# Optimization experiments

Measured on AMD Instinct MI355X. Metric: run time of the kernel, lower is better.

The kernel has to match this reference:

```python
import jax, jax.numpy as jnp
import numpy as np


def setup_inputs() -> dict:
    key = jax.random.key(0)
    k1, k2, k3, k4 = jax.random.split(key, 4)
    B, T, H = 4, 512, 256
    scale = 1.0 / np.sqrt(H)
    return {
        "rnn_outputs": jax.random.normal(k1, (B, T, H), dtype=jnp.float32),
        "W1": jax.random.normal(k2, (H, H), dtype=jnp.float32) * scale,
        "W2": jax.random.normal(k3, (H, H), dtype=jnp.float32) * scale,
        "v": jax.random.normal(k4, (H,), dtype=jnp.float32) * scale,
    }


def reference(rnn_outputs, W1, W2, v):
    """Bahdanau additive self-attention with causal mask.

    rnn_outputs: (B, T, H). Returns (context (B,T,H), weights (B,T,T)).
    """
    B, T, H = rnn_outputs.shape
    # nn.Linear applies x @ W.T
    query = rnn_outputs @ W1.T            # (B, T, H)
    keys = rnn_outputs @ W2.T             # (B, T, H)
    # scores[b,t,s] = v . tanh(q[b,t] + k[b,s]); materializes (B,T,T,H) like the original
    scores = jnp.einsum(
        "btsh,h->bts", jnp.tanh(query[:, :, None, :] + keys[:, None, :, :]), v
    )
    causal = jnp.triu(jnp.ones((T, T), dtype=bool), k=1)  # mask future positions
    scores = jnp.where(causal[None], -jnp.inf, scores)
    weights = jax.nn.softmax(scores, axis=-1)
    weights = jnp.nan_to_num(weights)
    context = jnp.einsum("bts,bsh->bth", weights, rnn_outputs)
    return context, weights
```

## Files before the change

### kernel.cpp

```cpp
#include <hip/hip_runtime.h>

namespace {

constexpr int kB = 4;
constexpr int kT = 512;
constexpr int kH = 256;

__device__ __forceinline__ float rcpf(float x) {
  return __builtin_amdgcn_rcpf(x);
}

__global__ __launch_bounds__(256) void transpose_w_kernel(
    const float* __restrict__ W1, const float* __restrict__ W2,
    float* __restrict__ Wt1, float* __restrict__ Wt2) {
  __shared__ float tile[32][33];
  const float* Win = (blockIdx.z == 0) ? W1 : W2;
  float* Wout = (blockIdx.z == 0) ? Wt1 : Wt2;
  const int jo = blockIdx.x * 32, ho = blockIdx.y * 32;
  const int c = threadIdx.x & 31, r0 = threadIdx.x >> 5;
#pragma unroll
  for (int p = 0; p < 4; ++p)
    tile[r0 + 8 * p][c] = Win[(size_t)(ho + r0 + 8 * p) * kH + jo + c];
  __syncthreads();
#pragma unroll
  for (int p = 0; p < 4; ++p)
    Wout[(size_t)(jo + r0 + 8 * p) * kH + ho + c] = tile[c][r0 + 8 * p];
}

__global__ __launch_bounds__(256) void proj_kernel(
    const float* __restrict__ X, const float* __restrict__ Wt1,
    const float* __restrict__ Wt2, float* __restrict__ EQt,
    float* __restrict__ EKt) {
  __shared__ __align__(16) float ws4[4][16][kH];

  const int tid = threadIdx.x;
  const int w = tid >> 6, lane = tid & 63;
  const int row0 = blockIdx.x * 8;
  const float* Wt = (blockIdx.y == 0) ? Wt1 : Wt2;
  float* dst = (blockIdx.y == 0) ? EQt : EKt;

  const float* gw = Wt + (size_t)(4 * w) * kH + lane * 4;

#define PSTAGE(buf, c)                                                       \
  {                                                                          \
    const size_t go = (size_t)(c) * 16 * kH;                                 \
    __builtin_amdgcn_global_load_lds(                                        \
        (const __attribute__((address_space(1))) void*)(gw + go),            \
        (__attribute__((address_space(3))) void*)&ws4[buf][4 * w][0], 16, 0, \
        0);                                                                  \
    __builtin_amdgcn_global_load_lds(                                        \
        (const __attribute__((address_space(1))) void*)(gw + go + kH),       \
        (__attribute__((address_space(3))) void*)&ws4[buf][4 * w + 1][0], 16,\
        0, 0);                                                               \
    __builtin_amdgcn_global_load_lds(                                        \
        (const __attribute__((address_space(1))) void*)(gw + go + 2 * kH),   \
        (__attribute__((address_space(3))) void*)&ws4[buf][4 * w + 2][0], 16,\
        0, 0);                                                               \
    __builtin_amdgcn_global_load_lds(                                        \
        (const __attribute__((address_space(1))) void*)(gw + go + 3 * kH),   \
        (__attribute__((address_space(3))) void*)&ws4[buf][4 * w + 3][0], 16,\
        0, 0);                                                               \
  }

  float acc[8];
#pragma unroll
  for (int i = 0; i < 8; ++i) acc[i] = 0.0f;

  PSTAGE(0, 0)
  PSTAGE(1, 1)
  PSTAGE(2, 2)

#pragma unroll 1
  for (int c = 0; c < 16; ++c) {
    if (c <= 13) {
      asm volatile("s_waitcnt vmcnt(8)" ::: "memory");
    } else if (c == 14) {
      asm volatile("s_waitcnt vmcnt(4)" ::: "memory");
    } else {
      asm volatile("s_waitcnt vmcnt(0)" ::: "memory");
    }
    __builtin_amdgcn_s_barrier();
    __builtin_amdgcn_sched_barrier(0);
    if (c <= 12) PSTAGE((c + 3) & 3, c + 3)
    const int bf = c & 3;
#pragma unroll
    for (int u = 0; u < 16; ++u) {
      const float wv = ws4[bf][u][tid];
#pragma unroll
      for (int i = 0; i < 8; ++i)
        acc[i] = __builtin_fmaf(X[(size_t)(row0 + i) * kH + c * 16 + u], wv,
                                acc[i]);
    }
  }
#undef PSTAGE

  const int bb = row0 >> 9, r0 = row0 & (kT - 1);
  float* out = dst + ((size_t)(bb * kH + tid)) * kT + r0;
  float4 lo = {__expf(2.0f * acc[0]), __expf(2.0f * acc[1]),
               __expf(2.0f * acc[2]), __expf(2.0f * acc[3])};
  float4 hi = {__expf(2.0f * acc[4]), __expf(2.0f * acc[5]),
               __expf(2.0f * acc[6]), __expf(2.0f * acc[7])};
  *reinterpret_cast<float4*>(out) = lo;
  *reinterpret_cast<float4*>(out + 4) = hi;
}

__global__ __launch_bounds__(256) void score_kernel(
    const float* __restrict__ EQt, const float* __restrict__ EKt,
    const float* __restrict__ v, float* __restrict__ Sc) {
  __shared__ __align__(16) float eqs[4][32 * 32];
  __shared__ __align__(16) float eks[4][32 * 32];

  const int tid = threadIdx.x;
  const int w = tid >> 6, lane = tid & 63;
  const int blk = blockIdx.x;
  const int xcd = blk & 7;
  const int b = xcd >> 1;
  const int tIdx = (xcd & 1) * 68 + (blk >> 3);

  int ti = (int)((__builtin_sqrtf(8.0f * (float)tIdx + 1.0f) - 1.0f) * 0.5f);
  while ((ti + 1) * (ti + 2) / 2 <= tIdx) ++ti;
  while (ti * (ti + 1) / 2 > tIdx) --ti;
  const int si = tIdx - ti * (ti + 1) / 2;
  const int t0 = ti * 32, s0 = si * 32;

  const int hoff = w * 8 + (lane >> 3);
  const int coff = (lane & 7) * 4;
  const float* gq = EQt + ((size_t)(b * kH + hoff) * kT) + t0 + coff;
  const float* gk = EKt + ((size_t)(b * kH + hoff) * kT) + s0 + coff;
  float* lqw = &eqs[0][0] + w * 256;
  float* lkw = &eks[0][0] + w * 256;

#define STAGE(buf, c)                                                        \
  {                                                                          \
    const size_t go = (size_t)(c) * 32 * kT;                                 \
    __builtin_amdgcn_global_load_lds(                                        \
        (const __attribute__((address_space(1))) void*)(gq + go),            \
        (__attribute__((address_space(3))) void*)(lqw + (buf)*1024), 16, 0,  \
        0);                                                                  \
    __builtin_amdgcn_global_load_lds(                                        \
        (const __attribute__((address_space(1))) void*)(gk + go),            \
        (__attribute__((address_space(3))) void*)(lkw + (buf)*1024), 16, 0,  \
        0);                                                                  \
  }

  const int wt = w >> 1, wsx = w & 1;
  const int tq = wt * 16 + 2 * (lane >> 3);
  const int sk = wsx * 16 + 2 * (lane & 7);

  float ac0 = 0.f, ac1 = 0.f, ac2 = 0.f, ac3 = 0.f;

  STAGE(0, 0)
  STAGE(1, 1)
  STAGE(2, 2)

#pragma unroll 1
  for (int c = 0; c < 8; ++c) {
    if (c <= 5) {
      asm volatile("s_waitcnt vmcnt(4)" ::: "memory");
    } else if (c == 6) {
      asm volatile("s_waitcnt vmcnt(2)" ::: "memory");
    } else {
      asm volatile("s_waitcnt vmcnt(0)" ::: "memory");
    }
    __builtin_amdgcn_s_barrier();
    __builtin_amdgcn_sched_barrier(0);
    if (c <= 4) STAGE((c + 3) & 3, c + 3)
    const int boff = (c & 3) * 1024;
    const float* vp = v + c * 32;
#pragma unroll
    for (int h = 0; h < 32; h += 2) {
      const float2 qA = *reinterpret_cast<const float2*>(&eqs[0][boff + h * 32 + tq]);
      const float2 kA = *reinterpret_cast<const float2*>(&eks[0][boff + h * 32 + sk]);
      const float2 qB = *reinterpret_cast<const float2*>(&eqs[0][boff + h * 32 + 32 + tq]);
      const float2 kB = *reinterpret_cast<const float2*>(&eks[0][boff + h * 32 + 32 + sk]);
      const float vA = vp[h], vB = vp[h + 1];
      {
        const float dA = __builtin_fmaf(qA.x, kA.x, 1.0f);
        const float dB = __builtin_fmaf(qB.x, kB.x, 1.0f);
        const float nm = __builtin_fmaf(vB, dA, vA * dB);
        ac0 = __builtin_fmaf(nm, rcpf(dA * dB), ac0);
      }
      {
        const float dA = __builtin_fmaf(qA.x, kA.y, 1.0f);
        const float dB = __builtin_fmaf(qB.x, kB.y, 1.0f);
        const float nm = __builtin_fmaf(vB, dA, vA * dB);
        ac1 = __builtin_fmaf(nm, rcpf(dA * dB), ac1);
      }
      {
        const float dA = __builtin_fmaf(qA.y, kA.x, 1.0f);
        const float dB = __builtin_fmaf(qB.y, kB.x, 1.0f);
        const float nm = __builtin_fmaf(vB, dA, vA * dB);
        ac2 = __builtin_fmaf(nm, rcpf(dA * dB), ac2);
      }
      {
        const float dA = __builtin_fmaf(qA.y, kA.y, 1.0f);
        const float dB = __builtin_fmaf(qB.y, kB.y, 1.0f);
        const float nm = __builtin_fmaf(vB, dA, vA * dB);
        ac3 = __builtin_fmaf(nm, rcpf(dA * dB), ac3);
      }
    }
  }
#undef STAGE

  float vv = v[lane] + v[lane + 64] + v[lane + 128] + v[lane + 192];
#pragma unroll
  for (int off = 32; off > 0; off >>= 1) vv += __shfl_xor(vv, off, 64);

  float2 row0v = {__builtin_fmaf(-2.0f, ac0, vv),
                  __builtin_fmaf(-2.0f, ac1, vv)};
  float2 row1v = {__builtin_fmaf(-2.0f, ac2, vv),
                  __builtin_fmaf(-2.0f, ac3, vv)};
  float* so = Sc + ((size_t)(b * kT + t0 + tq)) * kT + s0 + sk;
  *reinterpret_cast<float2*>(so) = row0v;
  *reinterpret_cast<float2*>(so + kT) = row1v;
}

__global__ __launch_bounds__(512) void attn2_kernel(
    const float* __restrict__ X, float* wsc, float* __restrict__ ctx) {
  __shared__ float wls[8][kT + 8];
  __shared__ __align__(16) float pc[8][8][kH];

  const int id = blockIdx.x;
  const int xcd = id & 7;
  const int b = xcd >> 1;
  const int sub = (xcd & 1) * 32 + (id >> 3);
  const int row0 = sub * 8;
  const int tid = threadIdx.x;
  const int w = tid >> 6, lane = tid & 63;

  const int t = row0 + w;
  float* srow = wsc + ((size_t)(b * kT + t)) * kT;
  const int sbase8 = lane * 8;
  float4 s4a = *reinterpret_cast<const float4*>(srow + sbase8);
  float4 s4b = *reinterpret_cast<const float4*>(srow + sbase8 + 4);
  float p[8];
  p[0] = (sbase8 + 0 <= t) ? __expf(s4a.x) : 0.f;
  p[1] = (sbase8 + 1 <= t) ? __expf(s4a.y) : 0.f;
  p[2] = (sbase8 + 2 <= t) ? __expf(s4a.z) : 0.f;
  p[3] = (sbase8 + 3 <= t) ? __expf(s4a.w) : 0.f;
  p[4] = (sbase8 + 4 <= t) ? __expf(s4b.x) : 0.f;
  p[5] = (sbase8 + 5 <= t) ? __expf(s4b.y) : 0.f;
  p[6] = (sbase8 + 6 <= t) ? __expf(s4b.z) : 0.f;
  p[7] = (sbase8 + 7 <= t) ? __expf(s4b.w) : 0.f;
  float l = ((p[0] + p[1]) + (p[2] + p[3])) + ((p[4] + p[5]) + (p[6] + p[7]));
#pragma unroll
  for (int off = 32; off > 0; off >>= 1) l += __shfl_xor(l, off, 64);
  const float rs = rcpf(l);
#pragma unroll
  for (int j = 0; j < 8; ++j) p[j] *= rs;
  float4 o4a = {p[0], p[1], p[2], p[3]};
  float4 o4b = {p[4], p[5], p[6], p[7]};
  *reinterpret_cast<float4*>(srow + sbase8) = o4a;
  *reinterpret_cast<float4*>(srow + sbase8 + 4) = o4b;
#pragma unroll
  for (int j = 0; j < 8; ++j) wls[w][sbase8 + j] = p[j];
  __syncthreads();

  const int h4 = lane * 4;
  const float* Xb = X + ((size_t)b * kT) * kH + h4;
  float4 acc4[8];
#pragma unroll
  for (int r = 0; r < 8; ++r) acc4[r] = {0.f, 0.f, 0.f, 0.f};

#pragma unroll 2
  for (int so = 0; so < 64; so += 4) {
    const int s = (w << 6) + so;
    const float4 x0 = *reinterpret_cast<const float4*>(Xb + (size_t)(s + 0) * kH);
    const float4 x1 = *reinterpret_cast<const float4*>(Xb + (size_t)(s + 1) * kH);
    const float4 x2 = *reinterpret_cast<const float4*>(Xb + (size_t)(s + 2) * kH);
    const float4 x3 = *reinterpret_cast<const float4*>(Xb + (size_t)(s + 3) * kH);
#pragma unroll
    for (int r = 0; r < 8; ++r) {
      const float4 wr = *reinterpret_cast<const float4*>(&wls[r][s]);
      float4 a = acc4[r];
      a.x = __builtin_fmaf(wr.x, x0.x, a.x);
      a.y = __builtin_fmaf(wr.x, x0.y, a.y);
      a.z = __builtin_fmaf(wr.x, x0.z, a.z);
      a.w = __builtin_fmaf(wr.x, x0.w, a.w);
      a.x = __builtin_fmaf(wr.y, x1.x, a.x);
      a.y = __builtin_fmaf(wr.y, x1.y, a.y);
      a.z = __builtin_fmaf(wr.y, x1.z, a.z);
      a.w = __builtin_fmaf(wr.y, x1.w, a.w);
      a.x = __builtin_fmaf(wr.z, x2.x, a.x);
      a.y = __builtin_fmaf(wr.z, x2.y, a.y);
      a.z = __builtin_fmaf(wr.z, x2.z, a.z);
      a.w = __builtin_fmaf(wr.z, x2.w, a.w);
      a.x = __builtin_fmaf(wr.w, x3.x, a.x);
      a.y = __builtin_fmaf(wr.w, x3.y, a.y);
      a.z = __builtin_fmaf(wr.w, x3.z, a.z);
      a.w = __builtin_fmaf(wr.w, x3.w, a.w);
      acc4[r] = a;
    }
  }
#pragma unroll
  for (int r = 0; r < 8; ++r)
    *reinterpret_cast<float4*>(&pc[w][r][h4]) = acc4[r];
  __syncthreads();

  float4 sum = {0.f, 0.f, 0.f, 0.f};
#pragma unroll
  for (int c = 0; c < 8; ++c) {
    const float4 q = *reinterpret_cast<const float4*>(&pc[c][w][h4]);
    sum.x += q.x;
    sum.y += q.y;
    sum.z += q.z;
    sum.w += q.w;
  }
  *reinterpret_cast<float4*>(
      ctx + ((size_t)(b * kT + row0 + w)) * kH + h4) = sum;
}

}

extern "C" void kernel_launch(void* const* d_in, const int* in_sizes, int n_in,
                              void* d_out, int out_size, void* d_ws,
                              size_t ws_size, hipStream_t stream) {
  const float* X = (const float*)d_in[0];
  const float* W1 = (const float*)d_in[1];
  const float* W2 = (const float*)d_in[2];
  const float* v = (const float*)d_in[3];

  float* ctx = (float*)d_out;
  float* wout = ctx + (size_t)kB * kT * kH;
  float* Wt1 = wout;
  float* Wt2 = wout + (size_t)kH * kH;
  float* Sc = wout;
  float* EQt = (float*)d_ws;
  float* EKt = EQt + (size_t)kB * kH * kT;

  transpose_w_kernel<<<dim3(8, 8, 2), 256, 0, stream>>>(W1, W2, Wt1, Wt2);
  proj_kernel<<<dim3(kB * kT / 8, 2), 256, 0, stream>>>(X, Wt1, Wt2, EQt, EKt);
  score_kernel<<<544, 256, 0, stream>>>(EQt, EKt, v, Sc);
  attn2_kernel<<<256, 512, 0, stream>>>(X, Sc, ctx);
}
```

Baseline: 60.69 us.

## Give each wave a private LDS slice in score kernel to drop barriers

```diff
diff --git a/kernel.cpp b/kernel.cpp
--- a/kernel.cpp
+++ b/kernel.cpp
@@ -107,8 +107,8 @@
 __global__ __launch_bounds__(256) void score_kernel(
     const float* __restrict__ EQt, const float* __restrict__ EKt,
     const float* __restrict__ v, float* __restrict__ Sc) {
-  __shared__ __align__(16) float eqs[4][32 * 32];
-  __shared__ __align__(16) float eks[4][32 * 32];
+  __shared__ __align__(16) float eqp[4][4][512];
+  __shared__ __align__(16) float ekp[4][4][512];
 
   const int tid = threadIdx.x;
   const int w = tid >> 6, lane = tid & 63;
@@ -123,29 +123,39 @@
   const int si = tIdx - ti * (ti + 1) / 2;
   const int t0 = ti * 32, s0 = si * 32;
 
-  const int hoff = w * 8 + (lane >> 3);
-  const int coff = (lane & 7) * 4;
-  const float* gq = EQt + ((size_t)(b * kH + hoff) * kT) + t0 + coff;
-  const float* gk = EKt + ((size_t)(b * kH + hoff) * kT) + s0 + coff;
-  float* lqw = &eqs[0][0] + w * 256;
-  float* lkw = &eks[0][0] + w * 256;
+  const int wt = w >> 1, wsx = w & 1;
+
+  const int hl = lane >> 2, cl = (lane & 3) * 4;
+  const float* gq =
+      EQt + ((size_t)(b * kH + hl) * kT) + t0 + 16 * wt + cl;
+  const float* gk =
+      EKt + ((size_t)(b * kH + hl) * kT) + s0 + 16 * wsx + cl;
+  float* eqw = &eqp[w][0][0];
+  float* ekw = &ekp[w][0][0];
 
 #define STAGE(buf, c)                                                        \
   {                                                                          \
     const size_t go = (size_t)(c) * 32 * kT;                                 \
     __builtin_amdgcn_global_load_lds(                                        \
         (const __attribute__((address_space(1))) void*)(gq + go),            \
-        (__attribute__((address_space(3))) void*)(lqw + (buf)*1024), 16, 0,  \
+        (__attribute__((address_space(3))) void*)(eqw + (buf)*512), 16, 0,   \
         0);                                                                  \
     __builtin_amdgcn_global_load_lds(                                        \
+        (const __attribute__((address_space(1))) void*)(gq + go + 16 * kT),  \
+        (__attribute__((address_space(3))) void*)(eqw + (buf)*512 + 256),    \
+        16, 0, 0);                                                           \
+    __builtin_amdgcn_global_load_lds(                                        \
         (const __attribute__((address_space(1))) void*)(gk + go),            \
-        (__attribute__((address_space(3))) void*)(lkw + (buf)*1024), 16, 0,  \
+        (__attribute__((address_space(3))) void*)(ekw + (buf)*512), 16, 0,   \
         0);                                                                  \
-  }
-
-  const int wt = w >> 1, wsx = w & 1;
-  const int tq = wt * 16 + 2 * (lane >> 3);
-  const int sk = wsx * 16 + 2 * (lane & 7);
+    __builtin_amdgcn_global_load_lds(                                        \
+        (const __attribute__((address_space(1))) void*)(gk + go + 16 * kT),  \
+        (__attribute__((address_space(3))) void*)(ekw + (buf)*512 + 256),    \
+        16, 0, 0);                                                           \
+  }
+
+  const int tq2 = 2 * (lane >> 3);
+  const int sk2 = 2 * (lane & 7);
 
   float ac0 = 0.f, ac1 = 0.f, ac2 = 0.f, ac3 = 0.f;
 
@@ -156,23 +166,26 @@
 #pragma unroll 1
   for (int c = 0; c < 8; ++c) {
     if (c <= 5) {
+      asm volatile("s_waitcnt vmcnt(8)" ::: "memory");
+    } else if (c == 6) {
       asm volatile("s_waitcnt vmcnt(4)" ::: "memory");
-    } else if (c == 6) {
-      asm volatile("s_waitcnt vmcnt(2)" ::: "memory");
     } else {
       asm volatile("s_waitcnt vmcnt(0)" ::: "memory");
     }
-    __builtin_amdgcn_s_barrier();
     __builtin_amdgcn_sched_barrier(0);
     if (c <= 4) STAGE((c + 3) & 3, c + 3)
-    const int boff = (c & 3) * 1024;
+    const int boff = (c & 3) * 512;
     const float* vp = v + c * 32;
 #pragma unroll
     for (int h = 0; h < 32; h += 2) {
-      const float2 qA = *reinterpret_cast<const float2*>(&eqs[0][boff + h * 32 + tq]);
-      const float2 kA = *reinterpret_cast<const float2*>(&eks[0][boff + h * 32 + sk]);
-      const float2 qB = *reinterpret_cast<const float2*>(&eqs[0][boff + h * 32 + 32 + tq]);
-      const float2 kB = *reinterpret_cast<const float2*>(&eks[0][boff + h * 32 + 32 + sk]);
+      const float2 qA =
+          *reinterpret_cast<const float2*>(&eqw[boff + h * 16 + tq2]);
+      const float2 kA =
+          *reinterpret_cast<const float2*>(&ekw[boff + h * 16 + sk2]);
+      const float2 qB =
+          *reinterpret_cast<const float2*>(&eqw[boff + h * 16 + 16 + tq2]);
+      const float2 kB =
+          *reinterpret_cast<const float2*>(&ekw[boff + h * 16 + 16 + sk2]);
       const float vA = vp[h], vB = vp[h + 1];
       {
         const float dA = __builtin_fmaf(qA.x, kA.x, 1.0f);
@@ -206,6 +219,8 @@
 #pragma unroll
   for (int off = 32; off > 0; off >>= 1) vv += __shfl_xor(vv, off, 64);
 
+  const int tq = wt * 16 + tq2;
+  const int sk = wsx * 16 + sk2;
   float2 row0v = {__builtin_fmaf(-2.0f, ac0, vv),
                   __builtin_fmaf(-2.0f, ac1, vv)};
   float2 row1v = {__builtin_fmaf(-2.0f, ac2, vv),
```

New measurement: 64.36 us. 1.06x slower.

## Stream X tiles into LDS with async global_load_lds ring buffer in attn2

Applied to the files above, without the earlier changes.

```diff
diff --git a/kernel.cpp b/kernel.cpp
--- a/kernel.cpp
+++ b/kernel.cpp
@@ -218,7 +218,7 @@
 __global__ __launch_bounds__(512) void attn2_kernel(
     const float* __restrict__ X, float* wsc, float* __restrict__ ctx) {
   __shared__ float wls[8][kT + 8];
-  __shared__ __align__(16) float pc[8][8][kH];
+  __shared__ __align__(16) float xr[4][16 * kH];
 
   const int id = blockIdx.x;
   const int xcd = id & 7;
@@ -254,60 +254,59 @@
   *reinterpret_cast<float4*>(srow + sbase8 + 4) = o4b;
 #pragma unroll
   for (int j = 0; j < 8; ++j) wls[w][sbase8 + j] = p[j];
-  __syncthreads();
 
   const int h4 = lane * 4;
-  const float* Xb = X + ((size_t)b * kT) * kH + h4;
-  float4 acc4[8];
-#pragma unroll
-  for (int r = 0; r < 8; ++r) acc4[r] = {0.f, 0.f, 0.f, 0.f};
-
-#pragma unroll 2
-  for (int so = 0; so < 64; so += 4) {
-    const int s = (w << 6) + so;
-    const float4 x0 = *reinterpret_cast<const float4*>(Xb + (size_t)(s + 0) * kH);
-    const float4 x1 = *reinterpret_cast<const float4*>(Xb + (size_t)(s + 1) * kH);
-    const float4 x2 = *reinterpret_cast<const float4*>(Xb + (size_t)(s + 2) * kH);
-    const float4 x3 = *reinterpret_cast<const float4*>(Xb + (size_t)(s + 3) * kH);
-#pragma unroll
-    for (int r = 0; r < 8; ++r) {
-      const float4 wr = *reinterpret_cast<const float4*>(&wls[r][s]);
-      float4 a = acc4[r];
-      a.x = __builtin_fmaf(wr.x, x0.x, a.x);
-      a.y = __builtin_fmaf(wr.x, x0.y, a.y);
-      a.z = __builtin_fmaf(wr.x, x0.z, a.z);
-      a.w = __builtin_fmaf(wr.x, x0.w, a.w);
-      a.x = __builtin_fmaf(wr.y, x1.x, a.x);
-      a.y = __builtin_fmaf(wr.y, x1.y, a.y);
-      a.z = __builtin_fmaf(wr.y, x1.z, a.z);
-      a.w = __builtin_fmaf(wr.y, x1.w, a.w);
-      a.x = __builtin_fmaf(wr.z, x2.x, a.x);
-      a.y = __builtin_fmaf(wr.z, x2.y, a.y);
-      a.z = __builtin_fmaf(wr.z, x2.z, a.z);
-      a.w = __builtin_fmaf(wr.z, x2.w, a.w);
-      a.x = __builtin_fmaf(wr.w, x3.x, a.x);
-      a.y = __builtin_fmaf(wr.w, x3.y, a.y);
-      a.z = __builtin_fmaf(wr.w, x3.z, a.z);
-      a.w = __builtin_fmaf(wr.w, x3.w, a.w);
-      acc4[r] = a;
-    }
-  }
-#pragma unroll
-  for (int r = 0; r < 8; ++r)
-    *reinterpret_cast<float4*>(&pc[w][r][h4]) = acc4[r];
-  __syncthreads();
-
-  float4 sum = {0.f, 0.f, 0.f, 0.f};
-#pragma unroll
-  for (int c = 0; c < 8; ++c) {
-    const float4 q = *reinterpret_cast<const float4*>(&pc[c][w][h4]);
-    sum.x += q.x;
-    sum.y += q.y;
-    sum.z += q.z;
-    sum.w += q.w;
-  }
+  const float* gx = X + ((size_t)b * kT) * kH + h4;
+
+#define XSTAGE(buf, c)                                                       \
+  {                                                                          \
+    const int sl0 = 2 * w;                                                   \
+    __builtin_amdgcn_global_load_lds(                                        \
+        (const __attribute__((address_space(1))) void*)(                     \
+            gx + (size_t)((c)*16 + sl0) * kH),                               \
+        (__attribute__((address_space(3))) void*)(&xr[buf][sl0 * kH]), 16,   \
+        0, 0);                                                               \
+    __builtin_amdgcn_global_load_lds(                                        \
+        (const __attribute__((address_space(1))) void*)(                     \
+            gx + (size_t)((c)*16 + sl0 + 1) * kH),                           \
+        (__attribute__((address_space(3))) void*)(&xr[buf][(sl0 + 1) * kH]), \
+        16, 0, 0);                                                           \
+  }
+
+  float4 acc = {0.f, 0.f, 0.f, 0.f};
+
+  XSTAGE(0, 0)
+  XSTAGE(1, 1)
+  XSTAGE(2, 2)
+
+#pragma unroll 1
+  for (int c = 0; c < 32; ++c) {
+    if (c <= 29) {
+      asm volatile("s_waitcnt vmcnt(4)" ::: "memory");
+    } else if (c == 30) {
+      asm volatile("s_waitcnt vmcnt(2)" ::: "memory");
+    } else {
+      asm volatile("s_waitcnt vmcnt(0)" ::: "memory");
+    }
+    __builtin_amdgcn_s_barrier();
+    __builtin_amdgcn_sched_barrier(0);
+    if (c <= 28) XSTAGE((c + 3) & 3, c + 3)
+    const int bf = c & 3;
+#pragma unroll 4
+    for (int sl = 0; sl < 16; ++sl) {
+      const float4 xv =
+          *reinterpret_cast<const float4*>(&xr[bf][sl * kH + h4]);
+      const float wt = wls[w][c * 16 + sl];
+      acc.x = __builtin_fmaf(wt, xv.x, acc.x);
+      acc.y = __builtin_fmaf(wt, xv.y, acc.y);
+      acc.z = __builtin_fmaf(wt, xv.z, acc.z);
+      acc.w = __builtin_fmaf(wt, xv.w, acc.w);
+    }
+  }
+#undef XSTAGE
+
   *reinterpret_cast<float4*>(
-      ctx + ((size_t)(b * kT + row0 + w)) * kH + h4) = sum;
+      ctx + ((size_t)(b * kT + row0 + w)) * kH + h4) = acc;
 }
 
 }
```

New measurement: 71.13 us. 1.17x slower.
